# Kernel tuning notes

Hardware: AMD Instinct MI355X
Metric: run time of the kernel (lower is better)

The kernel has to match this reference:

```python
import math
import jax, jax.numpy as jnp
import numpy as np

B = 2
TMAX = 1024
D = 1024
H = 16
DK = D // H
F = 4096
L = 2
CHUNK = 128
LEFT = 128
RIGHT = 32
EPS = 1e-5


def _build_mask(t_max, chunk, left, right):
    """Replicates EmformerEncoder.create_mask with audio_lens == t_max.
    Returns bool [T, T] where True = masked (disallowed), T = total_right + t_max."""
    num_chunks = math.ceil(t_max / chunk)
    ub = (num_chunks - 1) * right
    body = np.zeros((t_max, t_max), np.float32)
    mleft = np.zeros((t_max, ub), np.float32)
    mdiag = np.zeros((ub, ub), np.float32)
    mright = np.zeros((ub, t_max), np.float32)
    right_indexes = []
    for i in range(num_chunks):
        left_off = max(chunk * i - left, 0)
        start = chunk * i
        end = min(chunk * (i + 1), t_max)
        body[start:end, left_off:end] = 1
        if i == num_chunks - 1:
            break
        rem = t_max - (end + right)
        trl = right if rem >= 0 else t_max - end
        ri = len(right_indexes)
        mleft[start:start + chunk, ri:ri + trl] = 1
        mdiag[ri:ri + trl, ri:ri + trl] = 1
        mright[ri:ri + trl, left_off:end] = 1
        right_indexes += list(range(end, end + trl))
    rs = len(right_indexes)
    mleft = mleft[:, :rs]
    mdiag = mdiag[:rs, :rs]
    mright = mright[:rs, :]
    top = np.concatenate([mdiag, mright], axis=-1)
    bot = np.concatenate([mleft, body], axis=-1)
    m = np.concatenate([top, bot], axis=0)
    return m == 0  # True where attention is NOT allowed


def setup_inputs() -> dict:
    key = jax.random.key(0)
    ks = jax.random.split(key, 8)
    mask2d = _build_mask(TMAX, CHUNK, LEFT, RIGHT)  # [T, T]
    T = mask2d.shape[0]  # 1248
    w = lambda k, shape: jax.random.normal(k, shape, jnp.float32) * 0.02
    inp = {
        "input": jax.random.normal(ks[0], (B, T, D), jnp.float32),
        "ln_in_scale": jnp.ones((L, D), jnp.float32),
        "ln_in_bias": jnp.zeros((L, D), jnp.float32),
        "Wq": w(ks[1], (L, D, D)), "bq": jnp.zeros((L, D), jnp.float32),
        "Wk": w(ks[2], (L, D, D)), "bk": jnp.zeros((L, D), jnp.float32),
        "Wv": w(ks[3], (L, D, D)), "bv": jnp.zeros((L, D), jnp.float32),
        "ln1_scale": jnp.ones((L, D), jnp.float32),
        "ln1_bias": jnp.zeros((L, D), jnp.float32),
        "W1": w(ks[4], (L, D, F)), "b1": jnp.zeros((L, F), jnp.float32),
        "W2": w(ks[5], (L, F, D)), "b2": jnp.zeros((L, D), jnp.float32),
        "ln2_scale": jnp.ones((L, D), jnp.float32),
        "ln2_bias": jnp.zeros((L, D), jnp.float32),
        "mask": jnp.asarray(np.broadcast_to(mask2d[None, None], (B, 1, T, T)).copy()),
    }
    return inp


def _ln(x, scale, bias):
    m = jnp.mean(x, axis=-1, keepdims=True)
    v = jnp.mean(jnp.square(x - m), axis=-1, keepdims=True)
    return (x - m) * jax.lax.rsqrt(v + EPS) * scale + bias


def reference(input, ln_in_scale, ln_in_bias, Wq, bq, Wk, bk, Wv, bv,
              ln1_scale, ln1_bias, W1, b1, W2, b2, ln2_scale, ln2_bias, mask):
    x = input
    Bx, T, _ = x.shape
    scale = 1.0 / math.sqrt(DK)
    for l in range(L):
        h = _ln(x, ln_in_scale[l], ln_in_bias[l])  # pre-LN input (also residual base)
        q = (h @ Wq[l] + bq[l]).reshape(Bx, T, H, DK)
        k = (h @ Wk[l] + bk[l]).reshape(Bx, T, H, DK)
        v = (h @ Wv[l] + bv[l]).reshape(Bx, T, H, DK)
        scores = jnp.einsum('bqhd,bkhd->bhqk', q, k) * scale  # [B,H,T,T]
        scores = jnp.where(mask, -jnp.inf, scores)
        probs = jax.nn.softmax(scores, axis=-1)
        probs = jnp.where(mask, 0.0, probs)  # dropout_attn=0 -> identity
        o = jnp.einsum('bhqk,bkhd->bqhd', probs, v).reshape(Bx, T, D)
        attn_out = o + h
        y = _ln(attn_out, ln1_scale[l], ln1_bias[l])
        y = y @ W1[l] + b1[l]          # note: no activation in original code
        y = y @ W2[l] + b2[l] + attn_out
        x = _ln(y, ln2_scale[l], ln2_bias[l])
    return x
```

## Files before the change

### kernel.cpp

```cpp
#include <hip/hip_runtime.h>
#include <stdint.h>

typedef __attribute__((ext_vector_type(8))) short short8;
typedef __attribute__((ext_vector_type(4))) float f32x4;

#define DEV __device__ __forceinline__

DEV float bits2f(uint32_t u){ union{uint32_t u;float f;}v; v.u=u; return v.f; }
DEV float bf1(uint16_t s){ return bits2f(((uint32_t)s)<<16); }
DEV uint16_t f2bf(float f){ union{float f;uint32_t u;}v; v.f=f; uint32_t u=v.u;
  return (uint16_t)((u + 0x7fffu + ((u>>16)&1u))>>16); }
DEV uint16_t f2h(float a){ union{_Float16 h; uint16_t u;}v; v.h=(_Float16)a; return v.u; }
DEV float h2f(uint16_t s){ union{uint16_t u; _Float16 h;}v; v.u=s; return (float)v.h; }

DEV float ldval(const float* p, size_t i){ return p[i]; }
DEV float ldval(const uint16_t* p, size_t i){ return bf1(p[i]); }
DEV void stval(float* p, size_t i, float v){ p[i]=v; }
DEV void stval(uint16_t* p, size_t i, float v){ p[i]=f2bf(v); }

DEV void async16(const void* g, void* l){
#if __has_builtin(__builtin_amdgcn_global_load_lds)
  __builtin_amdgcn_global_load_lds((const __attribute__((address_space(1))) void*)g,
                                   (__attribute__((address_space(3))) void*)l, 16, 0, 0);
#else
  int lane = threadIdx.x & 63;
  *(uint4*)((char*)l + lane*16) = *(const uint4*)((const char*)g);
#endif
}

template<int TM, int TN, bool SPLIT>
__global__ __launch_bounds__(256) void gemm_t(
    const uint16_t* __restrict__ A, const uint16_t* __restrict__ Bt,
    const float* __restrict__ bias, void* __restrict__ Cout,
    int N, int K, int kchunk, int gm) {
  __shared__ uint16_t sA[3][TM*32];
  __shared__ uint16_t sB[3][TN*32];
  constexpr int LPS = TM/64 + TN/64;
  const int lin = blockIdx.y*gridDim.x + blockIdx.x;
  int mt_, nt_;
  if (gm > 0) {
    const int xcd = lin & 7, idx = lin >> 3;
    const int RM = gridDim.y / gm;
    const int RN = (gridDim.x * gm) >> 3;
    const int rm = xcd % gm, rn = xcd / gm;
    mt_ = rm*RM + idx % RM;
    nt_ = rn*RN + idx / RM;
  } else {
    const int q8 = (gridDim.x*gridDim.y) >> 3;
    const int swz = (lin & 7)*q8 + (lin >> 3);
    mt_ = swz % gridDim.y; nt_ = swz / gridDim.y;
  }
  const int m0 = mt_*TM, n0 = nt_*TN;
  const int kb = SPLIT ? blockIdx.z*kchunk : 0;
  const int kend = SPLIT ? kb + kchunk : K;
  const int tid = threadIdx.x, wid = tid>>6, lane = tid&63;
  constexpr int WM = TM/2, MT = WM/16;
  constexpr int WN = TN/2, NT = WN/16;
  const int wm = (wid&1)*WM, wn = (wid>>1)*WN;
  f32x4 acc[MT][NT];
  #pragma unroll
  for (int a=0;a<MT;a++)
    #pragma unroll
    for (int b=0;b<NT;b++) acc[a][b] = (f32x4){0.f,0.f,0.f,0.f};
  const int lrow = lane>>2;
  const int lcol = (((lane&3) ^ ((lrow>>1)&3)))*8;
  const int fr = lane&15, fc = lane>>4;
  const int rsw = (fc ^ ((fr>>1)&3))*8;

  auto stage = [&](int buf, int k0) {
    #pragma unroll
    for (int j = 0; j < TM/64; ++j) {
      int r0 = wid*(TM/4) + j*16;
      async16(A + (size_t)(m0+r0+lrow)*K + k0 + lcol, &sA[buf][r0*32]);
    }
    #pragma unroll
    for (int j = 0; j < TN/64; ++j) {
      int r0 = wid*(TN/4) + j*16;
      async16(Bt + (size_t)(n0+r0+lrow)*K + k0 + lcol, &sB[buf][r0*32]);
    }
  };

  const int niter = (kend - kb) >> 5;
  stage(0, kb);
  if (niter > 1) stage(1, kb + 32);
  int cur = 0;
  for (int it = 0; it < niter; ++it) {
    if (it+1 < niter) {
      if constexpr (LPS == 4)      asm volatile("s_waitcnt vmcnt(4)" ::: "memory");
      else if constexpr (LPS == 3) asm volatile("s_waitcnt vmcnt(3)" ::: "memory");
      else                         asm volatile("s_waitcnt vmcnt(2)" ::: "memory");
    } else {
      asm volatile("s_waitcnt vmcnt(0)" ::: "memory");
    }
    __builtin_amdgcn_s_barrier();
    __builtin_amdgcn_sched_barrier(0);
    if (it+2 < niter) {
      int b2 = cur+2; if (b2>=3) b2-=3;
      stage(b2, kb + (it+2)*32);
    }
    short8 af[MT], bfv[NT];
    #pragma unroll
    for (int t=0;t<MT;t++) af[t] = *(const short8*)&sA[cur][(wm + t*16 + fr)*32 + rsw];
    #pragma unroll
    for (int t=0;t<NT;t++) bfv[t] = *(const short8*)&sB[cur][(wn + t*16 + fr)*32 + rsw];
    #pragma unroll
    for (int mt=0;mt<MT;mt++)
      #pragma unroll
      for (int nt=0;nt<NT;nt++)
        acc[mt][nt] = __builtin_amdgcn_mfma_f32_16x16x32_bf16(af[mt], bfv[nt], acc[mt][nt], 0,0,0);
    if (++cur == 3) cur = 0;
  }
  const int cl = lane&15, rl = (lane>>4)*4;
  if (SPLIT) {
    float* Pz = (float*)Cout + (size_t)blockIdx.z*2560*N;
    #pragma unroll
    for (int nt=0;nt<NT;nt++) {
      int n = n0 + wn + nt*16 + cl;
      #pragma unroll
      for (int mt=0;mt<MT;mt++)
        #pragma unroll
        for (int r=0;r<4;r++)
          Pz[(size_t)(m0 + wm + mt*16 + rl + r)*N + n] = acc[mt][nt][r];
    }
  } else {
    uint16_t* C = (uint16_t*)Cout;
    #pragma unroll
    for (int nt=0;nt<NT;nt++) {
      int n = n0 + wn + nt*16 + cl;
      float bv = bias ? bias[n] : 0.f;
      #pragma unroll
      for (int mt=0;mt<MT;mt++)
        #pragma unroll
        for (int r=0;r<4;r++)
          C[(size_t)(m0 + wm + mt*16 + rl + r)*N + n] = f2bf(acc[mt][nt][r] + bv);
    }
  }
}

template<typename TI, typename TO>
DEV void ln_body(int row, int tid, const TI* x, const float* sc, const float* bi,
                 TO* out, float* red) {
  const size_t base = (size_t)row*1024 + tid*4;
  float v0=ldval(x,base), v1=ldval(x,base+1), v2=ldval(x,base+2), v3=ldval(x,base+3);
  float s = v0+v1+v2+v3;
  float sq = v0*v0+v1*v1+v2*v2+v3*v3;
  #pragma unroll
  for (int off=32; off; off>>=1){ s += __shfl_xor(s,off); sq += __shfl_xor(sq,off); }
  int wid=tid>>6, lane=tid&63;
  if (lane==0){ red[wid]=s; red[4+wid]=sq; }
  __syncthreads();
  s = red[0]+red[1]+red[2]+red[3]; sq = red[4]+red[5]+red[6]+red[7];
  float mean = s*(1.f/1024.f);
  float inv  = rsqrtf(sq*(1.f/1024.f) - mean*mean + 1e-5f);
  int c = tid*4;
  stval(out, base,   (v0-mean)*inv*sc[c]   + bi[c]);
  stval(out, base+1, (v1-mean)*inv*sc[c+1] + bi[c+1]);
  stval(out, base+2, (v2-mean)*inv*sc[c+2] + bi[c+2]);
  stval(out, base+3, (v3-mean)*inv*sc[c+3] + bi[c+3]);
}

template<typename TI, typename TO>
__global__ __launch_bounds__(256) void ln_k(const TI* __restrict__ x,
    const float* __restrict__ sc, const float* __restrict__ bi,
    TO* __restrict__ out) {
  __shared__ float red[8];
  ln_body<TI,TO>(blockIdx.x, threadIdx.x, x, sc, bi, out, red);
}

template<typename TO>
__global__ __launch_bounds__(256) void ln2_fused(const float* __restrict__ P,
    const float* __restrict__ b2, const uint16_t* __restrict__ resid,
    const float* __restrict__ sc, const float* __restrict__ bi,
    TO* __restrict__ out) {
  const int row = blockIdx.x, tid = threadIdx.x;
  const size_t base = (size_t)row*1024 + tid*4;
  float4 p0 = *(const float4*)(P + base);
  float4 p1 = *(const float4*)(P + (size_t)2560*1024 + base);
  int c = tid*4;
  float v0 = p0.x+p1.x+b2[c]  +bf1(resid[base]);
  float v1 = p0.y+p1.y+b2[c+1]+bf1(resid[base+1]);
  float v2 = p0.z+p1.z+b2[c+2]+bf1(resid[base+2]);
  float v3 = p0.w+p1.w+b2[c+3]+bf1(resid[base+3]);
  float s = v0+v1+v2+v3;
  float sq = v0*v0+v1*v1+v2*v2+v3*v3;
  #pragma unroll
  for (int off=32; off; off>>=1){ s += __shfl_xor(s,off); sq += __shfl_xor(sq,off); }
  __shared__ float red[8];
  int wid=tid>>6, lane=tid&63;
  if (lane==0){ red[wid]=s; red[4+wid]=sq; }
  __syncthreads();
  s = red[0]+red[1]+red[2]+red[3]; sq = red[4]+red[5]+red[6]+red[7];
  float mean = s*(1.f/1024.f);
  float inv  = rsqrtf(sq*(1.f/1024.f) - mean*mean + 1e-5f);
  stval(out, base,   (v0-mean)*inv*sc[c]   + bi[c]);
  stval(out, base+1, (v1-mean)*inv*sc[c+1] + bi[c+1]);
  stval(out, base+2, (v2-mean)*inv*sc[c+2] + bi[c+2]);
  stval(out, base+3, (v3-mean)*inv*sc[c+3] + bi[c+3]);
}

__global__ __launch_bounds__(256) void attn_fused(
    const uint32_t* __restrict__ qkv32, const uint16_t* __restrict__ hres,
    uint16_t* __restrict__ attn_out) {
  const int blk = blockIdx.x;
  const int qg = blk & 3, ci = (blk>>2)&7, hh = (blk>>5)&15, bb = blk>>9;
  const int sum_cnt = (ci<7)?32:0;
  const int bstart = (ci>=1)?128*(ci-1):0;
  const int bend = (ci==7)?1024:128*(ci+1);
  const int nk = sum_cnt + (bend - bstart);
  const int rowbase = bb*1248;
  const int tid = threadIdx.x, wid = tid>>6, lane = tid&63;
  const int fr = lane&15, fc = lane>>4;

  __shared__ __attribute__((aligned(16))) uint16_t sm[30848];
  uint16_t* K16 = sm;
  uint32_t* KD  = (uint32_t*)sm;
  uint16_t* Q16 = sm + 20736;
  uint32_t* QD  = KD + 10368;
  uint16_t* SP16 = sm;
  uint16_t* V16 = sm + 11840;
  uint32_t* VD  = (uint32_t*)(sm + 11840);

  for (int idx = tid; idx < nk*8; idx += 256) {
    int j = idx>>3, q4 = idx&7;
    int tk = (j < sum_cnt) ? (32*ci + j) : (224 + bstart + (j - sum_cnt));
    *(uint4*)&KD[j*36 + q4*4] =
      *(const uint4*)&qkv32[(size_t)(rowbase+tk)*1536 + 512 + hh*32 + q4*4];
  }
  for (int idx = tid; idx < 40*8; idx += 256) {
    int j = idx>>3, q4 = idx&7;
    int ql = qg*40 + j;
    int tq = (ql<32) ? (32*ci+ql) : (224+128*ci+ql-32);
    *(uint4*)&QD[j*36 + q4*4] =
      *(const uint4*)&qkv32[(size_t)(rowbase+tq)*1536 + hh*32 + q4*4];
  }
  __syncthreads();

  const int n_mt = nk>>4;
  const int qoff[3] = {0,16,24};
  f32x4 accs[5][3];
  #pragma unroll
  for (int a=0;a<5;a++)
    #pragma unroll
    for (int b=0;b<3;b++) accs[a][b] = (f32x4){0.f,0.f,0.f,0.f};
  __builtin_amdgcn_s_setprio(1);
  #pragma unroll
  for (int ks=0; ks<2; ++ks) {
    short8 bq_[3];
    #pragma unroll
    for (int nt=0;nt<3;nt++)
      bq_[nt] = *(const short8*)&Q16[(qoff[nt]+fr)*72 + ks*32 + fc*8];
    #pragma unroll
    for (int t=0;t<5;t++) {
      int mt = wid + 4*t;
      if (mt < n_mt) {
        short8 a_ = *(const short8*)&K16[(mt*16+fr)*72 + ks*32 + fc*8];
        #pragma unroll
        for (int nt=0;nt<3;nt++)
          accs[t][nt] = __builtin_amdgcn_mfma_f32_16x16x32_bf16(a_, bq_[nt], accs[t][nt], 0,0,0);
      }
    }
  }
  __builtin_amdgcn_s_setprio(0);
  __syncthreads();

  #pragma unroll
  for (int t=0;t<5;t++) {
    int mt = wid + 4*t;
    if (mt < n_mt) {
      #pragma unroll
      for (int nt=0;nt<3;nt++) {
        int q = qoff[nt] + fr;
        #pragma unroll
        for (int r=0;r<4;r++)
          SP16[q*296 + mt*16 + fc*4 + r] = f2h(accs[t][nt][r]*0.125f);
      }
    }
  }
  for (int idx = tid; idx < nk*8; idx += 256) {
    int j = idx>>3, q4 = idx&7;
    int tk = (j < sum_cnt) ? (32*ci + j) : (224 + bstart + (j - sum_cnt));
    uint4 w = *(const uint4*)&qkv32[(size_t)(rowbase+tk)*1536 + 1024 + hh*32 + q4*4];
    uint32_t* dst = &VD[j*33 + q4*4];
    dst[0]=w.x; dst[1]=w.y; dst[2]=w.z; dst[3]=w.w;
  }
  __syncthreads();

  for (int i=0;i<10;i++) {
    int row = wid*10 + i;
    float v[5];
    #pragma unroll
    for (int g=0;g<5;g++){ int k=g*64+lane; v[g] = (k<nk) ? h2f(SP16[row*296+k]) : -1e30f; }
    float mx = fmaxf(fmaxf(fmaxf(v[0],v[1]),fmaxf(v[2],v[3])),v[4]);
    #pragma unroll
    for (int off=32; off; off>>=1) mx = fmaxf(mx, __shfl_xor(mx,off));
    float p[5], sum=0.f;
    #pragma unroll
    for (int g=0;g<5;g++){ p[g] = __expf(v[g]-mx); if (g*64+lane>=nk) p[g]=0.f; sum+=p[g]; }
    #pragma unroll
    for (int off=32; off; off>>=1) sum += __shfl_xor(sum,off);
    float inv = 1.f/sum;
    #pragma unroll
    for (int g=0;g<5;g++){ int k=g*64+lane; if (k<nk) SP16[row*296+k] = f2bf(p[g]*inv); }
  }
  __syncthreads();

  const int nkt = nk>>5;
  f32x4 acco[3];
  #pragma unroll
  for (int t=0;t<3;t++) acco[t] = (f32x4){0.f,0.f,0.f,0.f};
  const uint16_t* vcol = V16 + wid*16 + fr;
  __builtin_amdgcn_s_setprio(1);
  for (int kt=0; kt<nkt; ++kt) {
    short8 bv_;
    #pragma unroll
    for (int j=0;j<8;j++) bv_[j] = (short)vcol[(kt*32 + fc*8 + j)*66];
    #pragma unroll
    for (int t=0;t<3;t++) {
      short8 a_ = *(const short8*)&SP16[(qoff[t]+fr)*296 + kt*32 + fc*8];
      acco[t] = __builtin_amdgcn_mfma_f32_16x16x32_bf16(a_, bv_, acco[t], 0,0,0);
    }
  }
  __builtin_amdgcn_s_setprio(0);
  #pragma unroll
  for (int t=0;t<3;t++) {
    #pragma unroll
    for (int r=0;r<4;r++) {
      bool vq = true;
      if (ci==7 && qg==0 && (qoff[t]+fc*4+r)<32) vq = false;
      if (vq) {
        int qll = qg*40 + qoff[t] + fc*4 + r;
        int tq = (qll<32) ? (32*ci+qll) : (224+128*ci+qll-32);
        size_t addr = (size_t)(rowbase+tq)*1024 + hh*64 + wid*16 + fr;
        attn_out[addr] = f2bf(acco[t][r] + bf1(hres[addr]));
      }
    }
  }
}

__global__ void prep_k(const float* __restrict__ Wq, const float* __restrict__ Wk,
                       const float* __restrict__ Wv, const float* __restrict__ W1,
                       const float* __restrict__ W2, const float* __restrict__ bq,
                       const float* __restrict__ bk, const float* __restrict__ bv,
                       uint16_t* __restrict__ wt_qkv, uint16_t* __restrict__ wt_w1,
                       uint16_t* __restrict__ wt_w2, float* __restrict__ bqkv,
                       const void* __restrict__ lnx, int lnx_f32,
                       const float* __restrict__ lnsc, const float* __restrict__ lnbi,
                       uint16_t* __restrict__ lnout) {
  __shared__ float t[32][33];
  const int blk = blockIdx.x;
  const int tx = threadIdx.x, ty = threadIdx.y;
  if (blk >= 11276) {
    int row = blk - 11276;
    int tid = ty*32 + tx;
    float* red = &t[0][0];
    if (lnx_f32) ln_body<float,uint16_t>((int)row, tid, (const float*)lnx, lnsc, lnbi, lnout, red);
    else         ln_body<uint16_t,uint16_t>((int)row, tid, (const uint16_t*)lnx, lnsc, lnbi, lnout, red);
    return;
  }
  if (blk >= 11264) {
    int i = (blk-11264)*256 + ty*32 + tx;
    bqkv[i] = (i<1024) ? bq[i] : ((i<2048) ? bk[i-1024] : bv[i-2048]);
    return;
  }
  const float* src; uint16_t* dst; int R, C, c0, r0;
  if (blk < 3072) {
    int w = blk>>10, tt = blk&1023;
    src = (w==0)?Wq:((w==1)?Wk:Wv); dst = wt_qkv + (size_t)w*1048576;
    R = 1024; C = 1024; c0 = (tt&31)*32; r0 = (tt>>5)*32;
  } else if (blk < 7168) {
    int tt = blk-3072;
    src = W1; dst = wt_w1; R = 1024; C = 4096;
    c0 = (tt&127)*32; r0 = (tt>>7)*32;
  } else {
    int tt = blk-7168;
    src = W2; dst = wt_w2; R = 4096; C = 1024;
    c0 = (tt&31)*32; r0 = (tt>>5)*32;
  }
  #pragma unroll
  for (int i=0;i<4;i++) t[ty+8*i][tx] = src[(size_t)(r0+ty+8*i)*C + c0+tx];
  __syncthreads();
  #pragma unroll
  for (int i=0;i<4;i++) dst[(size_t)(c0+ty+8*i)*R + r0+tx] = f2bf(t[tx][ty+8*i]);
}

extern "C" void kernel_launch(void* const* d_in, const int* in_sizes, int n_in,
                              void* d_out, int out_size, void* d_ws, size_t ws_size,
                              hipStream_t stream) {
  const float* input  = (const float*)d_in[0];
  const float* lnin_s = (const float*)d_in[1];
  const float* lnin_b = (const float*)d_in[2];
  const float* Wq = (const float*)d_in[3];
  const float* bq = (const float*)d_in[4];
  const float* Wk = (const float*)d_in[5];
  const float* bk = (const float*)d_in[6];
  const float* Wv = (const float*)d_in[7];
  const float* bv = (const float*)d_in[8];
  const float* ln1_s = (const float*)d_in[9];
  const float* ln1_b = (const float*)d_in[10];
  const float* W1 = (const float*)d_in[11];
  const float* b1 = (const float*)d_in[12];
  const float* W2 = (const float*)d_in[13];
  const float* b2 = (const float*)d_in[14];
  const float* ln2_s = (const float*)d_in[15];
  const float* ln2_b = (const float*)d_in[16];

  char* ws = (char*)d_ws;
  uint16_t* wt_qkv = (uint16_t*)(ws + 0);
  uint16_t* wt_w1  = (uint16_t*)(ws + 6291456);
  uint16_t* wt_w2  = (uint16_t*)(ws + 14680064);
  float*    bqkv   = (float*)   (ws + 23068672);
  uint16_t* hbuf   = (uint16_t*)(ws + 23080960);
  uint16_t* qkvb   = (uint16_t*)(ws + 28323840);
  uint16_t* attnb  = (uint16_t*)(ws + 44052480);
  uint16_t* zbuf   = (uint16_t*)(ws + 49295360);
  float*    pbuf   = (float*)   (ws + 54538240);
  uint16_t* y1b    = hbuf;
  uint16_t* x1b    = zbuf;

  const uint16_t* xcur_bf = x1b;
  for (int l=0; l<2; ++l) {
    prep_k<<<13772, dim3(32,8), 0, stream>>>(Wq+(size_t)l*1048576, Wk+(size_t)l*1048576,
        Wv+(size_t)l*1048576, W1+(size_t)l*4194304, W2+(size_t)l*4194304,
        bq+l*1024, bk+l*1024, bv+l*1024, wt_qkv, wt_w1, wt_w2, bqkv,
        (l==0) ? (const void*)input : (const void*)xcur_bf, (l==0)?1:0,
        lnin_s+l*1024, lnin_b+l*1024, hbuf);

    gemm_t<128,128,false><<<dim3(24,20),256,0,stream>>>(hbuf, wt_qkv, bqkv, qkvb, 3072, 1024, 1024, 2);
    attn_fused<<<1024,256,0,stream>>>((const uint32_t*)qkvb, hbuf, attnb);
    ln_k<uint16_t,uint16_t><<<2496,256,0,stream>>>(attnb, ln1_s+l*1024, ln1_b+l*1024, zbuf);
    gemm_t<128,128,false><<<dim3(32,20),256,0,stream>>>(zbuf, wt_w1, b1+l*4096, y1b, 4096, 1024, 1024, 2);
    gemm_t<128,64,true><<<dim3(16,20,2),256,0,stream>>>(y1b, wt_w2, nullptr, pbuf, 1024, 4096, 2048, 0);
    if (l==1) ln2_fused<float>   <<<2496,256,0,stream>>>(pbuf, b2+l*1024, attnb, ln2_s+l*1024, ln2_b+l*1024, (float*)d_out);
    else      ln2_fused<uint16_t><<<2496,256,0,stream>>>(pbuf, b2+l*1024, attnb, ln2_s+l*1024, ln2_b+l*1024, x1b);
  }
  (void)in_sizes; (void)n_in; (void)out_size; (void)ws_size;
}
```

Before: 483.9 us.

## Fold W1/W2 transpose into QKV GEMM launch and remap attention block order

The W1/W2 fp32-to-bf16 transposes move out of prep_k and run as extra blocks appended to the QKV GEMM grid. Those blocks can then overlap with the GEMM tiles instead of sitting on the critical path before the QKV GEMM. The grid is flattened to 1D, and the GEMM tile swizzle now uses explicit gx/gy instead of gridDim. The attention kernel's block index is remapped so the four query groups of one (chunk, head) are spaced 8 apart, likely to spread them across XCDs, but they may then lose shared K/V cache locality.

After: 481.8 us. No clear change (-0.4%).

```diff
diff --git a/kernel.cpp b/kernel.cpp
--- a/kernel.cpp
+++ b/kernel.cpp
@@ -32,28 +32,49 @@
 __global__ __launch_bounds__(256) void gemm_t(
     const uint16_t* __restrict__ A, const uint16_t* __restrict__ Bt,
     const float* __restrict__ bias, void* __restrict__ Cout,
-    int N, int K, int kchunk, int gm) {
+    int N, int K, int kchunk, int gm, int gx, int gy, int nG,
+    const float* __restrict__ Tsrc1, const float* __restrict__ Tsrc2,
+    uint16_t* __restrict__ Tdst1, uint16_t* __restrict__ Tdst2) {
   __shared__ uint16_t sA[3][TM*32];
   __shared__ uint16_t sB[3][TN*32];
   constexpr int LPS = TM/64 + TN/64;
-  const int lin = blockIdx.y*gridDim.x + blockIdx.x;
+  const int tid = threadIdx.x;
+  const int lin = blockIdx.y*gx + blockIdx.x;
+
+  if (lin >= nG) {
+    float (*t)[33] = (float(*)[33])&sA[0][0];
+    int tt = lin - nG;
+    const float* src; uint16_t* dst; int R, C, c0, r0;
+    if (tt < 4096) { src = Tsrc1; dst = Tdst1; R = 1024; C = 4096;
+                     c0 = (tt&127)*32; r0 = (tt>>7)*32; }
+    else { tt -= 4096; src = Tsrc2; dst = Tdst2; R = 4096; C = 1024;
+           c0 = (tt&31)*32; r0 = (tt>>5)*32; }
+    const int tx = tid&31, ty = tid>>5;
+    #pragma unroll
+    for (int i=0;i<4;i++) t[ty+8*i][tx] = src[(size_t)(r0+ty+8*i)*C + c0+tx];
+    __syncthreads();
+    #pragma unroll
+    for (int i=0;i<4;i++) dst[(size_t)(c0+ty+8*i)*R + r0+tx] = f2bf(t[tx][ty+8*i]);
+    return;
+  }
+
   int mt_, nt_;
   if (gm > 0) {
     const int xcd = lin & 7, idx = lin >> 3;
-    const int RM = gridDim.y / gm;
-    const int RN = (gridDim.x * gm) >> 3;
+    const int RM = gy / gm;
+    const int RN = (gx * gm) >> 3;
     const int rm = xcd % gm, rn = xcd / gm;
     mt_ = rm*RM + idx % RM;
     nt_ = rn*RN + idx / RM;
   } else {
-    const int q8 = (gridDim.x*gridDim.y) >> 3;
+    const int q8 = (gx*gy) >> 3;
     const int swz = (lin & 7)*q8 + (lin >> 3);
-    mt_ = swz % gridDim.y; nt_ = swz / gridDim.y;
+    mt_ = swz % gy; nt_ = swz / gy;
   }
   const int m0 = mt_*TM, n0 = nt_*TN;
   const int kb = SPLIT ? blockIdx.z*kchunk : 0;
   const int kend = SPLIT ? kb + kchunk : K;
-  const int tid = threadIdx.x, wid = tid>>6, lane = tid&63;
+  const int wid = tid>>6, lane = tid&63;
   constexpr int WM = TM/2, MT = WM/16;
   constexpr int WN = TN/2, NT = WN/16;
   const int wm = (wid&1)*WM, wn = (wid>>1)*WN;
@@ -202,7 +223,9 @@
     const uint32_t* __restrict__ qkv32, const uint16_t* __restrict__ hres,
     uint16_t* __restrict__ attn_out) {
   const int blk = blockIdx.x;
-  const int qg = blk & 3, ci = (blk>>2)&7, hh = (blk>>5)&15, bb = blk>>9;
+  const int qg = (blk>>3)&3;
+  const int g  = (blk&7) + ((blk>>5)<<3);
+  const int ci = g&7, hh = (g>>3)&15, bb = g>>7;
   const int sum_cnt = (ci<7)?32:0;
   const int bstart = (ci>=1)?128*(ci-1):0;
   const int bend = (ci==7)?1024:128*(ci+1);
@@ -289,18 +312,18 @@
     int row = wid*10 + i;
     float v[5];
     #pragma unroll
-    for (int g=0;g<5;g++){ int k=g*64+lane; v[g] = (k<nk) ? h2f(SP16[row*296+k]) : -1e30f; }
+    for (int g2=0;g2<5;g2++){ int k=g2*64+lane; v[g2] = (k<nk) ? h2f(SP16[row*296+k]) : -1e30f; }
     float mx = fmaxf(fmaxf(fmaxf(v[0],v[1]),fmaxf(v[2],v[3])),v[4]);
     #pragma unroll
     for (int off=32; off; off>>=1) mx = fmaxf(mx, __shfl_xor(mx,off));
     float p[5], sum=0.f;
     #pragma unroll
-    for (int g=0;g<5;g++){ p[g] = __expf(v[g]-mx); if (g*64+lane>=nk) p[g]=0.f; sum+=p[g]; }
+    for (int g2=0;g2<5;g2++){ p[g2] = __expf(v[g2]-mx); if (g2*64+lane>=nk) p[g2]=0.f; sum+=p[g2]; }
     #pragma unroll
     for (int off=32; off; off>>=1) sum += __shfl_xor(sum,off);
     float inv = 1.f/sum;
     #pragma unroll
-    for (int g=0;g<5;g++){ int k=g*64+lane; if (k<nk) SP16[row*296+k] = f2bf(p[g]*inv); }
+    for (int g2=0;g2<5;g2++){ int k=g2*64+lane; if (k<nk) SP16[row*296+k] = f2bf(p[g2]*inv); }
   }
   __syncthreads();
 
@@ -338,44 +361,33 @@
 }
 
 __global__ void prep_k(const float* __restrict__ Wq, const float* __restrict__ Wk,
-                       const float* __restrict__ Wv, const float* __restrict__ W1,
-                       const float* __restrict__ W2, const float* __restrict__ bq,
+                       const float* __restrict__ Wv, const float* __restrict__ bq,
                        const float* __restrict__ bk, const float* __restrict__ bv,
-                       uint16_t* __restrict__ wt_qkv, uint16_t* __restrict__ wt_w1,
-                       uint16_t* __restrict__ wt_w2, float* __restrict__ bqkv,
+                       uint16_t* __restrict__ wt_qkv, float* __restrict__ bqkv,
                        const void* __restrict__ lnx, int lnx_f32,
                        const float* __restrict__ lnsc, const float* __restrict__ lnbi,
                        uint16_t* __restrict__ lnout) {
   __shared__ float t[32][33];
   const int blk = blockIdx.x;
   const int tx = threadIdx.x, ty = threadIdx.y;
-  if (blk >= 11276) {
-    int row = blk - 11276;
+  if (blk >= 3084) {
+    int row = blk - 3084;
     int tid = ty*32 + tx;
     float* red = &t[0][0];
     if (lnx_f32) ln_body<float,uint16_t>((int)row, tid, (const float*)lnx, lnsc, lnbi, lnout, red);
     else         ln_body<uint16_t,uint16_t>((int)row, tid, (const uint16_t*)lnx, lnsc, lnbi, lnout, red);
     return;
   }
-  if (blk >= 11264) {
-    int i = (blk-11264)*256 + ty*32 + tx;
+  if (blk >= 3072) {
+    int i = (blk-3072)*256 + ty*32 + tx;
     bqkv[i] = (i<1024) ? bq[i] : ((i<2048) ? bk[i-1024] : bv[i-2048]);
     return;
   }
-  const float* src; uint16_t* dst; int R, C, c0, r0;
-  if (blk < 3072) {
-    int w = blk>>10, tt = blk&1023;
-    src = (w==0)?Wq:((w==1)?Wk:Wv); dst = wt_qkv + (size_t)w*1048576;
-    R = 1024; C = 1024; c0 = (tt&31)*32; r0 = (tt>>5)*32;
-  } else if (blk < 7168) {
-    int tt = blk-3072;
-    src = W1; dst = wt_w1; R = 1024; C = 4096;
-    c0 = (tt&127)*32; r0 = (tt>>7)*32;
-  } else {
-    int tt = blk-7168;
-    src = W2; dst = wt_w2; R = 4096; C = 1024;
-    c0 = (tt&31)*32; r0 = (tt>>5)*32;
-  }
+  int w = blk>>10, tt = blk&1023;
+  const float* src = (w==0)?Wq:((w==1)?Wk:Wv);
+  uint16_t* dst = wt_qkv + (size_t)w*1048576;
+  const int R = 1024, C = 1024;
+  const int c0 = (tt&31)*32, r0 = (tt>>5)*32;
   #pragma unroll
   for (int i=0;i<4;i++) t[ty+8*i][tx] = src[(size_t)(r0+ty+8*i)*C + c0+tx];
   __syncthreads();
@@ -419,17 +431,20 @@
 
   const uint16_t* xcur_bf = x1b;
   for (int l=0; l<2; ++l) {
-    prep_k<<<13772, dim3(32,8), 0, stream>>>(Wq+(size_t)l*1048576, Wk+(size_t)l*1048576,
-        Wv+(size_t)l*1048576, W1+(size_t)l*4194304, W2+(size_t)l*4194304,
-        bq+l*1024, bk+l*1024, bv+l*1024, wt_qkv, wt_w1, wt_w2, bqkv,
+    prep_k<<<5580, dim3(32,8), 0, stream>>>(Wq+(size_t)l*1048576, Wk+(size_t)l*1048576,
+        Wv+(size_t)l*1048576, bq+l*1024, bk+l*1024, bv+l*1024, wt_qkv, bqkv,
         (l==0) ? (const void*)input : (const void*)xcur_bf, (l==0)?1:0,
         lnin_s+l*1024, lnin_b+l*1024, hbuf);
 
-    gemm_t<128,128,false><<<dim3(24,20),256,0,stream>>>(hbuf, wt_qkv, bqkv, qkvb, 3072, 1024, 1024, 2);
+    gemm_t<128,128,false><<<dim3(8672),256,0,stream>>>(hbuf, wt_qkv, bqkv, qkvb,
+        3072, 1024, 0, 2, 24, 20, 480,
+        W1+(size_t)l*4194304, W2+(size_t)l*4194304, wt_w1, wt_w2);
     attn_fused<<<1024,256,0,stream>>>((const uint32_t*)qkvb, hbuf, attnb);
     ln_k<uint16_t,uint16_t><<<2496,256,0,stream>>>(attnb, ln1_s+l*1024, ln1_b+l*1024, zbuf);
-    gemm_t<128,128,false><<<dim3(32,20),256,0,stream>>>(zbuf, wt_w1, b1+l*4096, y1b, 4096, 1024, 1024, 2);
-    gemm_t<128,64,true><<<dim3(16,20,2),256,0,stream>>>(y1b, wt_w2, nullptr, pbuf, 1024, 4096, 2048, 0);
+    gemm_t<128,128,false><<<dim3(32,20),256,0,stream>>>(zbuf, wt_w1, b1+l*4096, y1b,
+        4096, 1024, 0, 2, 32, 20, 640, nullptr, nullptr, nullptr, nullptr);
+    gemm_t<128,64,true><<<dim3(16,20,2),256,0,stream>>>(y1b, wt_w2, nullptr, pbuf,
+        1024, 4096, 2048, 0, 16, 20, 320, nullptr, nullptr, nullptr, nullptr);
     if (l==1) ln2_fused<float>   <<<2496,256,0,stream>>>(pbuf, b2+l*1024, attnb, ln2_s+l*1024, ln2_b+l*1024, (float*)d_out);
     else      ln2_fused<uint16_t><<<2496,256,0,stream>>>(pbuf, b2+l*1024, attnb, ln2_s+l*1024, ln2_b+l*1024, x1b);
   }
```
